# Performance work log

Hardware: AMD Instinct MI355X
Metric: run time of the kernel (lower is better)

Reference implementation:

```python
import jax, jax.numpy as jnp
import numpy as np

B, N, E, D = 2, 8192, 1024, 128   # batch, seq, embed_dim, expand_ratio (= head dim)
H = E // D                        # 8 heads (f_proj output dim)
CHUNK = 64
LN_EPS = 1e-5


def _gla_chunked(q, k, v, log_f):
    """Chunked simple GLA: S_t = exp(log_f_t) * S_{t-1} + k_t v_t^T ; o_t = q_t @ S_t.
    q,k,v: [b,h,n,d], log_f: [b,h,n] (log of per-head scalar decay in (0,1))."""
    b, h, n, d = q.shape
    nc = n // CHUNK
    qc = q.reshape(b, h, nc, CHUNK, d)
    kc = k.reshape(b, h, nc, CHUNK, d)
    vc = v.reshape(b, h, nc, CHUNK, d)
    gf = log_f.reshape(b, h, nc, CHUNK)
    g = jnp.cumsum(gf, axis=-1)          # inclusive within-chunk cum log decay [b,h,nc,C]
    gl = g[..., -1]                      # total chunk log decay [b,h,nc]

    # intra-chunk: A[i,j] = (q_i . k_j) * exp(g_i - g_j), j <= i  (g decreasing -> stable)
    mask = jnp.tril(jnp.ones((CHUNK, CHUNK), bool))
    A = jnp.einsum('bhcid,bhcjd->bhcij', qc, kc)
    A = jnp.where(mask, A * jnp.exp(g[..., :, None] - g[..., None, :]), 0.0)
    o_intra = jnp.einsum('bhcij,bhcjd->bhcid', A, vc)

    # inter-chunk: scan over chunks carrying state S [b,h,d,d]
    def step(S, inp):
        q_c, k_c, v_c, g_c, gl_c = inp   # [b,h,C,d],[b,h,C,d],[b,h,C,d],[b,h,C],[b,h]
        o = jnp.einsum('bhid,bhde->bhie', q_c * jnp.exp(g_c)[..., None], S)
        kd = k_c * jnp.exp(gl_c[..., None] - g_c)[..., None]
        S = jnp.exp(gl_c)[..., None, None] * S + jnp.einsum('bhid,bhie->bhde', kd, v_c)
        return S, o

    xs = (jnp.moveaxis(qc, 2, 0), jnp.moveaxis(kc, 2, 0), jnp.moveaxis(vc, 2, 0),
          jnp.moveaxis(g, 2, 0), jnp.moveaxis(gl, 2, 0))
    S0 = jnp.zeros((b, h, d, d), q.dtype)
    _, o_inter = jax.lax.scan(step, S0, xs)      # [nc,b,h,C,d]
    o_inter = jnp.moveaxis(o_inter, 0, 2)        # [b,h,nc,C,d]
    return (o_intra + o_inter).reshape(b, h, n, d)


def setup_inputs() -> dict:
    key = jax.random.key(0)
    ks = jax.random.split(key, 13)
    s = E ** -0.5
    x = jax.random.normal(ks[0], (B, N, E), jnp.float32)
    # per-head lower bound in (0,1), stored in log space as consumed by the module
    log_lower_bound = jnp.log(jax.random.uniform(ks[1], (H,), jnp.float32, 0.05, 0.95))
    Wq = jax.random.normal(ks[2], (E, E), jnp.float32) * s
    Wk = jax.random.normal(ks[3], (E, E), jnp.float32) * s
    Wv = jax.random.normal(ks[4], (E, E), jnp.float32) * s
    Wf = jax.random.normal(ks[5], (E, H), jnp.float32) * s
    Wb1 = jax.random.normal(ks[6], (E, D), jnp.float32) * s
    Wb2 = jax.random.normal(ks[7], (D, E), jnp.float32) * (D ** -0.5)
    Wg1 = jax.random.normal(ks[8], (E, D), jnp.float32) * s
    Wg2 = jax.random.normal(ks[9], (D, E), jnp.float32) * (D ** -0.5)
    Wo = jax.random.normal(ks[10], (E, E), jnp.float32) * s
    ln_scale = jnp.ones((E,), jnp.float32)
    ln_bias = jnp.zeros((E,), jnp.float32)
    return dict(x=x, log_lower_bound=log_lower_bound, Wq=Wq, Wk=Wk, Wv=Wv, Wf=Wf,
                Wb1=Wb1, Wb2=Wb2, Wg1=Wg1, Wg2=Wg2, Wo=Wo,
                ln_scale=ln_scale, ln_bias=ln_bias)


def reference(x, log_lower_bound, Wq, Wk, Wv, Wf, Wb1, Wb2, Wg1, Wg2, Wo, ln_scale, ln_bias):
    silu = jax.nn.silu
    q = silu(x @ Wq)
    k = silu(x @ Wk)
    v = x @ Wv
    f_pre = x @ Wf                               # [B,N,H] per-head decay logits

    # dense-memory Householder-style reflection of q
    beta = silu((x @ Wb1) @ Wb2)
    nb = jnp.sqrt(jnp.sum(beta * beta, axis=-1, keepdims=True))
    beta = beta / jnp.maximum(nb, 1e-6) / (E ** 0.5)
    q = q - 2.0 * jnp.sum(q * beta, axis=-1, keepdims=True) * beta

    def split(t):
        return t.reshape(B, N, H, D).transpose(0, 2, 1, 3)   # [B,H,N,D]
    qh, kh, vh = split(q), split(k), split(v)

    lb = jnp.exp(log_lower_bound)                            # [H]
    f = lb + (1.0 - lb) * jax.nn.sigmoid(f_pre)              # [B,N,H]
    log_f = jnp.log(f).transpose(0, 2, 1)                    # [B,H,N]

    o = _gla_chunked(qh, kh, vh, log_f)                      # [B,H,N,D]
    o = o.transpose(0, 2, 1, 3).reshape(B, N, E)

    gate = jax.nn.sigmoid((x @ Wg1) @ Wg2)
    o = o * gate

    mu = jnp.mean(o, axis=-1, keepdims=True)
    var = jnp.var(o, axis=-1, keepdims=True)
    o = (o - mu) / jnp.sqrt(var + LN_EPS) * ln_scale + ln_bias
    return o @ Wo
```

## Files before the change

### kernel.cpp

```cpp
#include <hip/hip_runtime.h>
#include <hip/hip_bf16.h>
#include <cstdint>


using u16 = unsigned short;
using u32 = unsigned int;
using u64 = unsigned long long;

typedef __attribute__((ext_vector_type(8))) short s16x8;
typedef __attribute__((ext_vector_type(4))) float f32x4;

__device__ __forceinline__ float b2f(u16 b){ u32 u = ((u32)b)<<16; return __builtin_bit_cast(float,u); }
__device__ __forceinline__ u16 f2b(float f){
  u32 u = __builtin_bit_cast(u32,f);
  return (u16)((u + 0x7FFFu + ((u>>16)&1u)) >> 16);
}
__device__ __forceinline__ float sigm(float x){ return 1.f/(1.f + __expf(-x)); }
__device__ __forceinline__ float silu(float x){ return x * sigm(x); }

__device__ __forceinline__ void gload16(const void* g, void* l){
  __builtin_amdgcn_global_load_lds((const __attribute__((address_space(1))) void*)g,
                                   (__attribute__((address_space(3))) void*)l, 16, 0, 0);
}
#define MFMA(a,b,c) __builtin_amdgcn_mfma_f32_16x16x32_bf16((a),(b),(c),0,0,0)

__device__ __forceinline__ void bar(){
  asm volatile("" ::: "memory");
  __builtin_amdgcn_s_barrier();
  asm volatile("" ::: "memory");
}
__device__ __forceinline__ void wait_vm8(){
  asm volatile("s_waitcnt vmcnt(8)" ::: "memory");
  __builtin_amdgcn_sched_barrier(0);
}
__device__ __forceinline__ void wait_vm0(){
  asm volatile("s_waitcnt vmcnt(0)" ::: "memory");
  __builtin_amdgcn_sched_barrier(0);
}

__device__ __forceinline__ void swz_block(int& bx, int& by){
  const int gx = gridDim.x;
  const int nwg = gx * gridDim.y;
  int lin = by*gx + bx;
  const int cpx = nwg >> 3;
  lin = (lin & 7)*cpx + (lin >> 3);
  bx = lin % gx; by = lin / gx;
}

__global__ __launch_bounds__(256) void fill_diag(float* __restrict__ p, int n, float val){
  int i = blockIdx.x*256 + threadIdx.x;
  if (i < n) p[i] = val;
}

__global__ __launch_bounds__(256) void wprep_all(const float* __restrict__ Wq,
                                                 const float* __restrict__ Wk,
                                                 const float* __restrict__ Wv,
                                                 const float* __restrict__ Wb1,
                                                 const float* __restrict__ Wb2,
                                                 const float* __restrict__ Wg1,
                                                 const float* __restrict__ Wg2,
                                                 const float* __restrict__ Wo,
                                                 u16* __restrict__ WCAT,
                                                 u16* __restrict__ WB2T,
                                                 u16* __restrict__ WG2T,
                                                 u16* __restrict__ WOT){
  const int z = blockIdx.z;
  const float* src; u16* dst; int K, Nsrc, kb, nb;
  switch(z){
    case 0: src=Wq;  dst=WCAT;            K=1024; Nsrc=1024; kb=16; nb=16; break;
    case 1: src=Wk;  dst=WCAT+1024*1024;  K=1024; Nsrc=1024; kb=16; nb=16; break;
    case 2: src=Wv;  dst=WCAT+2048*1024;  K=1024; Nsrc=1024; kb=16; nb=16; break;
    case 3: src=Wb1; dst=WCAT+3072*1024;  K=1024; Nsrc=128;  kb=16; nb=2;  break;
    case 4: src=Wg1; dst=WCAT+3200*1024;  K=1024; Nsrc=128;  kb=16; nb=2;  break;
    case 5: src=Wb2; dst=WB2T;            K=128;  Nsrc=1024; kb=2;  nb=16; break;
    case 6: src=Wg2; dst=WG2T;            K=128;  Nsrc=1024; kb=2;  nb=16; break;
    default:src=Wo;  dst=WOT;             K=1024; Nsrc=1024; kb=16; nb=16; break;
  }
  if (blockIdx.x >= (u32)kb || blockIdx.y >= (u32)nb) return;
  __shared__ float t[64][65];
  const int k0 = blockIdx.x*64, n0 = blockIdx.y*64;
  const int tid = threadIdx.x;
  #pragma unroll
  for (int e=0;e<16;e++){
    int idx = e*256 + tid;
    int r = idx>>6, c = idx&63;
    float v = 0.f;
    if (n0 + c < Nsrc) v = src[(u64)(k0+r)*Nsrc + n0 + c];
    t[r][c] = v;
  }
  __syncthreads();
  #pragma unroll
  for (int e=0;e<16;e++){
    int idx = e*256 + tid;
    int nn = idx>>6, kk = idx&63;
    dst[(u64)(n0+nn)*K + k0 + kk] = f2b(t[kk][nn]);
  }
}

__global__ __launch_bounds__(256) void fprep(const float* __restrict__ x,
                                             const float* __restrict__ Wf,
                                             const float* __restrict__ llb,
                                             float* __restrict__ G,
                                             float* __restrict__ GL,
                                             u16* __restrict__ XB){
  const int c = blockIdx.x, b = blockIdx.y;
  const int tid = threadIdx.x;
  __shared__ float wf[4*2056];
  __shared__ float fsm[64][8];
  for (int i = tid; i < 2048; i += 256){
    float4 v = ((const float4*)Wf)[i];
    const int dim = i>>1, half = i&1;
    const int q = dim>>8, r = dim&255;
    *(float4*)&wf[q*2056 + (r*2+half)*4] = v;
  }
  __syncthreads();
  const int t = tid>>2, q = tid&3;
  const u64 tokoff = (u64)(b*8192 + c*64 + t)*1024 + q*256;
  const float4* xr = (const float4*)(x + tokoff);
  ushort4* xbw = (ushort4*)(XB + tokoff);
  const float* wq = wf + q*2056;
  float4 s0 = {0,0,0,0}, s1 = {0,0,0,0};
  #pragma unroll 4
  for (int i=0;i<64;i++){
    const float4 xv = xr[i];
    ushort4 ob; ob.x=f2b(xv.x); ob.y=f2b(xv.y); ob.z=f2b(xv.z); ob.w=f2b(xv.w);
    xbw[i] = ob;
    const float* xe = (const float*)&xv;
    #pragma unroll
    for (int e=0;e<4;e++){
      const float4 w0 = *(const float4*)&wq[((i*4+e)*2+0)*4];
      const float4 w1 = *(const float4*)&wq[((i*4+e)*2+1)*4];
      s0.x += xe[e]*w0.x; s0.y += xe[e]*w0.y; s0.z += xe[e]*w0.z; s0.w += xe[e]*w0.w;
      s1.x += xe[e]*w1.x; s1.y += xe[e]*w1.y; s1.z += xe[e]*w1.z; s1.w += xe[e]*w1.w;
    }
  }
  #pragma unroll
  for (int d=1; d<4; d<<=1){
    s0.x += __shfl_xor(s0.x,d); s0.y += __shfl_xor(s0.y,d);
    s0.z += __shfl_xor(s0.z,d); s0.w += __shfl_xor(s0.w,d);
    s1.x += __shfl_xor(s1.x,d); s1.y += __shfl_xor(s1.y,d);
    s1.z += __shfl_xor(s1.z,d); s1.w += __shfl_xor(s1.w,d);
  }
  if (q==0){
    fsm[t][0]=s0.x; fsm[t][1]=s0.y; fsm[t][2]=s0.z; fsm[t][3]=s0.w;
    fsm[t][4]=s1.x; fsm[t][5]=s1.y; fsm[t][6]=s1.z; fsm[t][7]=s1.w;
  }
  __syncthreads();
  if (tid < 64){
    #pragma unroll
    for (int h=0;h<8;h++){
      const float lb = __expf(llb[h]);
      const float f = lb + (1.f - lb)*sigm(fsm[tid][h]);
      float xg = __logf(f);
      #pragma unroll
      for (int d=1; d<64; d<<=1){
        float v = __shfl_up(xg, d);
        if (tid >= d) xg += v;
      }
      const int bh = b*8 + h;
      G[(u64)bh*8192 + c*64 + tid] = xg;
      if (tid==63) GL[bh*128 + c] = xg;
    }
  }
}

__global__ __launch_bounds__(256,4) void gemm_proj(const u16* __restrict__ A,
                                                   const u16* __restrict__ Bt,
                                                   u16* __restrict__ Qb,
                                                   u16* __restrict__ Kp,
                                                   u16* __restrict__ KT,
                                                   u16* __restrict__ VT,
                                                   u16* __restrict__ FP,
                                                   const float* __restrict__ Gp,
                                                   const float* __restrict__ GLp){
  __shared__ __align__(16) u16 As[128*64];
  __shared__ __align__(16) u16 Bs[128*64];
  const int tid = threadIdx.x, lane = tid&63, wid = tid>>6;
  int bx = blockIdx.x, by = blockIdx.y;
  swz_block(bx, by);
  const int bn0 = bx*128, bm0 = by*128;
  const int wr = wid>>1, wc = wid&1;
  const int g = lane>>4, ln = lane&15;

  f32x4 acc[4][4];
  #pragma unroll
  for (int i=0;i<4;i++)
    #pragma unroll
    for (int j=0;j<4;j++) acc[i][j] = f32x4{0.f,0.f,0.f,0.f};

  for (int kt = 0; kt < 16; ++kt){
    const int k0 = kt<<6;
    #pragma unroll
    for (int j=0;j<4;j++){
      const int p = (wid*4+j)*64 + lane;
      const int row = p>>3, sl = p&7;
      const int sc = ((sl ^ (row&7))<<3);
      gload16(A  + (u64)(bm0+row)*1024 + k0 + sc, (char*)As + (wid*4+j)*1024);
      gload16(Bt + (u64)(bn0+row)*1024 + k0 + sc, (char*)Bs + (wid*4+j)*1024);
    }
    __syncthreads();
    #pragma unroll
    for (int ks=0;ks<2;ks++){
      s16x8 af[4], bf[4];
      #pragma unroll
      for (int mt=0;mt<4;mt++){
        const int row = wr*64 + mt*16 + ln;
        af[mt] = *(const s16x8*)(As + row*64 + (((ks*4+g) ^ (row&7))<<3));
      }
      #pragma unroll
      for (int nt=0;nt<4;nt++){
        const int row = wc*64 + nt*16 + ln;
        bf[nt] = *(const s16x8*)(Bs + row*64 + (((ks*4+g) ^ (row&7))<<3));
      }
      #pragma unroll
      for (int mt=0;mt<4;mt++)
        #pragma unroll
        for (int nt=0;nt<4;nt++)
          acc[mt][nt] = MFMA(af[mt], bf[nt], acc[mt][nt]);
    }
    __syncthreads();
  }

  const int cb = bn0 >> 7;
  if (cb < 8){
    #pragma unroll
    for (int mt=0;mt<4;mt++)
      #pragma unroll
      for (int nt=0;nt<4;nt++){
        const int col = bn0 + wc*64 + nt*16 + ln;
        #pragma unroll
        for (int r=0;r<4;r++)
          Qb[(u64)(bm0 + wr*64 + mt*16 + g*4 + r)*1024 + col] = f2b(acc[mt][nt][r]);
      }
  } else if (cb < 16){
    const int h = cb - 8;
    const int bh = (bm0>>13)*8 + h;
    const int trowb = (bm0 & 8191) + wr*64;
    const float gl = GLp[bh*128 + (trowb>>6)];
    float es[4][4];
    #pragma unroll
    for (int mt=0;mt<4;mt++)
      #pragma unroll
      for (int r=0;r<4;r++)
        es[mt][r] = __expf(gl - Gp[(u64)bh*8192 + trowb + mt*16 + g*4 + r]);
    #pragma unroll
    for (int mt=0;mt<4;mt++){
      const int trow = trowb + mt*16 + g*4;
      #pragma unroll
      for (int nt=0;nt<4;nt++){
        const int d = wc*64 + nt*16 + ln;
        ushort4 o; u16* op = (u16*)&o;
        #pragma unroll
        for (int r=0;r<4;r++){
          const float s = silu(acc[mt][nt][r]);
          op[r] = f2b(s * es[mt][r]);
          Kp[(u64)(bm0 + wr*64 + mt*16 + g*4 + r)*1024 + h*128 + d] = f2b(s);
        }
        *(ushort4*)(KT + ((u64)bh*128 + d)*8192 + trow) = o;
      }
    }
  } else if (cb < 24){
    const int h = cb - 16;
    const int bh = (bm0>>13)*8 + h;
    const int trowb = (bm0 & 8191) + wr*64;
    #pragma unroll
    for (int mt=0;mt<4;mt++){
      const int trow = trowb + mt*16 + g*4;
      #pragma unroll
      for (int nt=0;nt<4;nt++){
        const int d = wc*64 + nt*16 + ln;
        ushort4 o; u16* op = (u16*)&o;
        #pragma unroll
        for (int r=0;r<4;r++) op[r] = f2b(acc[mt][nt][r]);
        *(ushort4*)(VT + ((u64)bh*128 + d)*8192 + trow) = o;
      }
    }
  } else {
    const int off = (cb == 24) ? 0 : 128;
    #pragma unroll
    for (int mt=0;mt<4;mt++)
      #pragma unroll
      for (int nt=0;nt<4;nt++){
        const int col = off + wc*64 + nt*16 + ln;
        #pragma unroll
        for (int r=0;r<4;r++)
          FP[(u64)(bm0 + wr*64 + mt*16 + g*4 + r)*384 + col] = f2b(acc[mt][nt][r]);
      }
  }
}

#define STAGE256(kt_, c_)                                                              \
  do{ const int kk0 = (kt_)<<6;                                                        \
    _Pragma("unroll")                                                                  \
    for (int j=0;j<4;j++){                                                             \
      const int p = j*512 + tid;                                                       \
      const int row = p>>3, sl = p&7;                                                  \
      const int sc = ((sl ^ (row&7))<<3);                                              \
      gload16(A  + (u64)(bm0+row)*lda + kk0 + sc,                                      \
              (char*)lds + (c_)*65536 + (j*8+wid)*1024);                               \
      gload16(Bt + (u64)(bn0+row)*K   + kk0 + sc,                                      \
              (char*)lds + (c_)*65536 + 32768 + (j*8+wid)*1024);                       \
    } }while(0)

#define GEMM256_CORE()                                                                 \
  f32x4 acc[8][4];                                                                     \
  _Pragma("unroll")                                                                    \
  for (int i=0;i<8;i++)                                                                \
    _Pragma("unroll")                                                                  \
    for (int j=0;j<4;j++) acc[i][j] = f32x4{0.f,0.f,0.f,0.f};                          \
  const int nk = K >> 6;                                                               \
  STAGE256(0, 0);                                                                      \
  int cbuf = 0;                                                                        \
  for (int kt = 0; kt < nk; ++kt){                                                     \
    if (kt+1 < nk){ STAGE256(kt+1, cbuf^1); wait_vm8(); } else { wait_vm0(); }         \
    bar();                                                                             \
    const u16* As_c = lds + cbuf*32768;                                                \
    const u16* Bs_c = As_c + 16384;                                                    \
    s16x8 bfr[2][4];                                                                   \
    _Pragma("unroll")                                                                  \
    for (int ks=0;ks<2;ks++)                                                           \
      _Pragma("unroll")                                                                \
      for (int n=0;n<4;n++){                                                           \
        const int row = wc*64 + n*16 + ln;                                             \
        bfr[ks][n] = *(const s16x8*)(Bs_c + row*64 + (((ks*4+g) ^ (row&7))<<3));       \
      }                                                                                \
    _Pragma("unroll")                                                                  \
    for (int m=0;m<8;m++){                                                             \
      const int arow = wr*128 + m*16 + ln;                                             \
      _Pragma("unroll")                                                                \
      for (int ks=0;ks<2;ks++){                                                        \
        const s16x8 af = *(const s16x8*)(As_c + arow*64 + (((ks*4+g) ^ (arow&7))<<3)); \
        _Pragma("unroll")                                                              \
        for (int n=0;n<4;n++) acc[m][n] = MFMA(af, bfr[ks][n], acc[m][n]);             \
      }                                                                                \
    }                                                                                  \
    bar();                                                                             \
    cbuf ^= 1;                                                                         \
  }

__global__ __launch_bounds__(512,2) void gemm256(const u16* __restrict__ A, int lda,
                                                 const u16* __restrict__ Bt,
                                                 void* __restrict__ C, int ldc,
                                                 int K, int mode){
  __shared__ __align__(16) u16 lds[2*32768];
  const int tid = threadIdx.x, lane = tid&63, wid = tid>>6;
  int bx = blockIdx.x, by = blockIdx.y;
  swz_block(bx, by);
  const int bn0 = bx*256, bm0 = by*256;
  const int wr = wid>>2, wc = wid&3;
  const int g = lane>>4, ln = lane&15;
  GEMM256_CORE();
  if (mode == 0){
    float* Cf = (float*)C;
    #pragma unroll
    for (int m=0;m<8;m++)
      #pragma unroll
      for (int n=0;n<4;n++){
        const int col = bn0 + wc*64 + n*16 + ln;
        #pragma unroll
        for (int r=0;r<4;r++)
          Cf[(u64)(bm0 + wr*128 + m*16 + g*4 + r)*ldc + col] = acc[m][n][r];
      }
  } else {
    u16* Cb = (u16*)C;
    #pragma unroll
    for (int m=0;m<8;m++)
      #pragma unroll
      for (int n=0;n<4;n++){
        const int col = bn0 + wc*64 + n*16 + ln;
        #pragma unroll
        for (int r=0;r<4;r++)
          Cb[(u64)(bm0 + wr*128 + m*16 + g*4 + r)*ldc + col] = f2b(acc[m][n][r]);
      }
  }
}

__global__ __launch_bounds__(256) void e1_reflect(u16* __restrict__ Q,
                                                  const u16* __restrict__ BP){
  const u64 t = blockIdx.x;
  const int tid = threadIdx.x;
  __shared__ float red[8];
  u16* qrow = Q + t*1024;
  const u16* brow = BP + t*1024;
  ushort4 qv = ((const ushort4*)qrow)[tid];
  ushort4 bv = ((const ushort4*)brow)[tid];
  u16* qp = (u16*)&qv; const u16* bp = (const u16*)&bv;
  float q[4], bb[4];
  float s1 = 0.f, s2 = 0.f;
  #pragma unroll
  for (int j=0;j<4;j++){
    const float qq = silu(b2f(qp[j]));
    const float bbv = silu(b2f(bp[j]));
    q[j] = qq; bb[j] = bbv;
    s1 += bbv*bbv; s2 += qq*bbv;
  }
  #pragma unroll
  for (int d=1; d<64; d<<=1){ s1 += __shfl_xor(s1,d); s2 += __shfl_xor(s2,d); }
  const int wid = tid>>6, lane = tid&63;
  if (lane==0){ red[wid]=s1; red[4+wid]=s2; }
  __syncthreads();
  s1 = red[0]+red[1]+red[2]+red[3];
  s2 = red[4]+red[5]+red[6]+red[7];
  const float bs = 1.f/(fmaxf(sqrtf(s1), 1e-6f) * 32.f);
  const float coef = 2.f * s2 * bs * bs;
  #pragma unroll
  for (int j=0;j<4;j++) qp[j] = f2b(q[j] - coef*bb[j]);
  ((ushort4*)qrow)[tid] = qv;
}

__global__ __launch_bounds__(256,4) void g1_local(const u16* __restrict__ KT,
                                                  const u16* __restrict__ VT,
                                                  u16* __restrict__ LT){
  __shared__ __align__(16) u16 kts[128*64];
  __shared__ __align__(16) u16 vts[128*64];
  const int c = blockIdx.x, bh = blockIdx.y;
  const int tid = threadIdx.x, lane = tid&63, wid = tid>>6;
  const int g = lane>>4, ln = lane&15;
  #pragma unroll
  for (int j=0;j<4;j++){
    const int p = (wid*4+j)*64 + lane;
    const int row = p>>3, sl = p&7;
    const int sc = ((sl ^ (row&7))<<3);
    gload16(KT + ((u64)bh*128 + row)*8192 + (u64)c*64 + sc, (char*)kts + (wid*4+j)*1024);
    gload16(VT + ((u64)bh*128 + row)*8192 + (u64)c*64 + sc, (char*)vts + (wid*4+j)*1024);
  }
  __syncthreads();
  f32x4 acc[2][8];
  #pragma unroll
  for (int mt=0;mt<2;mt++)
    #pragma unroll
    for (int dt=0;dt<8;dt++) acc[mt][dt] = f32x4{0.f,0.f,0.f,0.f};
  #pragma unroll
  for (int kk=0;kk<2;kk++){
    s16x8 av[2];
    #pragma unroll
    for (int mt=0;mt<2;mt++){
      const int row = wid*32 + mt*16 + ln;
      av[mt] = *(const s16x8*)(vts + row*64 + (((kk*4+g) ^ (row&7))<<3));
    }
    #pragma unroll
    for (int dt=0;dt<8;dt++){
      const int row = dt*16 + ln;
      const s16x8 bk = *(const s16x8*)(kts + row*64 + (((kk*4+g) ^ (row&7))<<3));
      #pragma unroll
      for (int mt=0;mt<2;mt++) acc[mt][dt] = MFMA(av[mt], bk, acc[mt][dt]);
    }
  }
  u16* out = LT + ((u64)(bh*128 + c)<<14);
  #pragma unroll
  for (int mt=0;mt<2;mt++)
    #pragma unroll
    for (int dt=0;dt<8;dt++){
      const int d = dt*16 + ln;
      #pragma unroll
      for (int r=0;r<4;r++){
        const int n = wid*32 + mt*16 + g*4 + r;
        out[n*128 + d] = f2b(acc[mt][dt][r]);
      }
    }
}

__global__ __launch_bounds__(256) void g2_scan(u16* __restrict__ LS,
                                               const float* __restrict__ GL){
  __shared__ float egl[128];
  const int bh = blockIdx.y;
  if (threadIdx.x < 128) egl[threadIdx.x] = __expf(GL[bh*128 + threadIdx.x]);
  __syncthreads();
  const u64 e = (u64)blockIdx.x*256 + threadIdx.x;
  u16* P = LS + ((u64)bh<<21) + e;
  float s = 0.f;
  for (int c=0;c<128;c++){
    const float l = b2f(P[(u64)c<<14]);
    P[(u64)c<<14] = f2b(s);
    s = egl[c]*s + l;
  }
}

__global__ __launch_bounds__(256,2) void g3_out(const u16* __restrict__ Qb,
                                                const u16* __restrict__ Kp,
                                                const u16* __restrict__ VT,
                                                const u16* __restrict__ SBb,
                                                const float* __restrict__ Gb,
                                                u16* __restrict__ O){
  __shared__ __align__(16) u16 qs[64*128];
  __shared__ __align__(16) u16 ks[64*128];
  __shared__ __align__(16) u16 vts[128*64];
  __shared__ __align__(16) u16 sbs[64*128];
  __shared__ __align__(16) u16 Ast[4][16*64];
  __shared__ float gg[64];
  const int c = blockIdx.x, bh = blockIdx.y;
  const int b = bh>>3, h = bh&7;
  const int tid = threadIdx.x, lane = tid&63, wid = tid>>6;
  const int g = lane>>4, ln = lane&15;
  const u64 trow0 = (u64)b*8192 + (u64)c*64;

  if (tid < 64) gg[tid] = Gb[(u64)bh*8192 + c*64 + tid];

  const u16* sbbase = SBb + ((u64)(bh*128 + c)<<14);
  #pragma unroll
  for (int j=0;j<4;j++){
    const int p = (wid*4+j)*64 + lane;
    const int row = p>>4, sl = p&15;
    const int sc = ((sl ^ (row&7))<<3);
    gload16(Qb + (trow0 + row)*1024 + h*128 + sc, (char*)qs + (wid*4+j)*1024);
    gload16(Kp + (trow0 + row)*1024 + h*128 + sc, (char*)ks + (wid*4+j)*1024);
    const int row2 = p>>3, sl2 = p&7;
    gload16(VT + ((u64)bh*128 + row2)*8192 + (u64)c*64 + ((sl2 ^ (row2&7))<<3),
            (char*)vts + (wid*4+j)*1024);
    gload16(sbbase + row*128 + sc, (char*)sbs + (wid*4+j)*1024);
  }
  __syncthreads();

  f32x4 pa[4];
  #pragma unroll
  for (int jt=0;jt<4;jt++) pa[jt] = f32x4{0.f,0.f,0.f,0.f};
  #pragma unroll
  for (int kk=0;kk<4;kk++){
    const int arow = wid*16 + ln;
    const s16x8 aq = *(const s16x8*)(qs + arow*128 + (((kk*4+g) ^ (arow&7))<<3));
    #pragma unroll
    for (int jt=0;jt<4;jt++){
      const int brow = jt*16 + ln;
      const s16x8 bk = *(const s16x8*)(ks + brow*128 + (((kk*4+g) ^ (brow&7))<<3));
      pa[jt] = MFMA(aq, bk, pa[jt]);
    }
  }
  #pragma unroll
  for (int jt=0;jt<4;jt++){
    const int jj = jt*16 + ln;
    const float gj = gg[jj];
    #pragma unroll
    for (int r=0;r<4;r++){
      const int il = g*4 + r;
      const int ii = wid*16 + il;
      const float v = (jj <= ii) ? pa[jt][r] * __expf(gg[ii] - gj) : 0.f;
      Ast[wid][il*64 + (((jj>>3) ^ (il&7))<<3) + (jj&7)] = f2b(v);
    }
  }
  {
    const int row = wid*16 + (lane>>2);
    const float sc = __expf(gg[row]);
    u16* base = qs + row*128 + (lane&3)*32;
    #pragma unroll
    for (int ee=0; ee<4; ee++){
      s16x8 v = *(s16x8*)(base + ee*8);
      u16* vp = (u16*)&v;
      #pragma unroll
      for (int xj=0;xj<8;xj++) vp[xj] = f2b(b2f(vp[xj]) * sc);
      *(s16x8*)(base + ee*8) = v;
    }
  }
  f32x4 acc[8];
  #pragma unroll
  for (int i=0;i<8;i++) acc[i] = f32x4{0.f,0.f,0.f,0.f};
  #pragma unroll
  for (int kk=0;kk<2;kk++){
    const s16x8 aa = *(const s16x8*)(Ast[wid] + ln*64 + (((kk*4+g) ^ (ln&7))<<3));
    #pragma unroll
    for (int nt=0;nt<8;nt++){
      const int brow = nt*16 + ln;
      const s16x8 bb = *(const s16x8*)(vts + brow*64 + (((kk*4+g) ^ (brow&7))<<3));
      acc[nt] = MFMA(aa, bb, acc[nt]);
    }
  }
  #pragma unroll
  for (int kk=0;kk<4;kk++){
    const int arow = wid*16 + ln;
    const s16x8 aq = *(const s16x8*)(qs + arow*128 + (((kk*4+g) ^ (arow&7))<<3));
    #pragma unroll
    for (int nt=0;nt<4;nt++){
      const int brow = nt*16 + ln;
      const s16x8 bs = *(const s16x8*)(sbs + brow*128 + (((kk*4+g) ^ (brow&7))<<3));
      acc[nt] = MFMA(aq, bs, acc[nt]);
    }
  }
  __syncthreads();
  #pragma unroll
  for (int j=0;j<4;j++){
    const int p = (wid*4+j)*64 + lane;
    const int row = p>>4, sl = p&15;
    gload16(sbbase + 8192 + row*128 + ((sl ^ (row&7))<<3), (char*)sbs + (wid*4+j)*1024);
  }
  __syncthreads();
  #pragma unroll
  for (int kk=0;kk<4;kk++){
    const int arow = wid*16 + ln;
    const s16x8 aq = *(const s16x8*)(qs + arow*128 + (((kk*4+g) ^ (arow&7))<<3));
    #pragma unroll
    for (int nt=0;nt<4;nt++){
      const int brow = nt*16 + ln;
      const s16x8 bs = *(const s16x8*)(sbs + brow*128 + (((kk*4+g) ^ (brow&7))<<3));
      acc[4+nt] = MFMA(aq, bs, acc[4+nt]);
    }
  }
  u16* outp = O + trow0*1024 + h*128;
  #pragma unroll
  for (int nt=0;nt<8;nt++){
    const int n = nt*16 + ln;
    #pragma unroll
    for (int r=0;r<4;r++){
      const int i = wid*16 + g*4 + r;
      outp[(u64)i*1024 + n] = f2b(acc[nt][r]);
    }
  }
}

__global__ __launch_bounds__(256) void e2_ln(const u16* __restrict__ O,
                                             const u16* __restrict__ GP,
                                             const float* __restrict__ lnsc,
                                             const float* __restrict__ lnbi,
                                             u16* __restrict__ OL){
  const u64 t = blockIdx.x;
  const int tid = threadIdx.x;
  __shared__ float red[8];
  ushort4 ov = ((const ushort4*)(O + t*1024))[tid];
  ushort4 gv = ((const ushort4*)(GP + t*1024))[tid];
  const u16* ovp = (const u16*)&ov;
  const u16* gvp = (const u16*)&gv;
  float o[4]; float s = 0.f, s2 = 0.f;
  #pragma unroll
  for (int j=0;j<4;j++){
    const float val = b2f(ovp[j]) * sigm(b2f(gvp[j]));
    o[j] = val; s += val; s2 += val*val;
  }
  #pragma unroll
  for (int d=1; d<64; d<<=1){ s += __shfl_xor(s,d); s2 += __shfl_xor(s2,d); }
  const int wid = tid>>6, lane = tid&63;
  if (lane==0){ red[wid]=s; red[4+wid]=s2; }
  __syncthreads();
  s = red[0]+red[1]+red[2]+red[3];
  s2 = red[4]+red[5]+red[6]+red[7];
  const float mu = s * (1.f/1024.f);
  const float var = s2 * (1.f/1024.f) - mu*mu;
  const float rs = rsqrtf(var + 1e-5f);
  ushort4 out; u16* op = (u16*)&out;
  #pragma unroll
  for (int j=0;j<4;j++){
    const int e = tid*4 + j;
    op[j] = f2b((o[j]-mu)*rs*lnsc[e] + lnbi[e]);
  }
  ((ushort4*)(OL + t*1024))[tid] = out;
}

extern "C" void kernel_launch(void* const* d_in, const int* in_sizes, int n_in,
                              void* d_out, int out_size, void* d_ws, size_t ws_size,
                              hipStream_t stream){
  const float* x   = (const float*)d_in[0];
  const float* llb = (const float*)d_in[1];
  const float* Wq  = (const float*)d_in[2];
  const float* Wk  = (const float*)d_in[3];
  const float* Wv  = (const float*)d_in[4];
  const float* Wf  = (const float*)d_in[5];
  const float* Wb1 = (const float*)d_in[6];
  const float* Wb2 = (const float*)d_in[7];
  const float* Wg1 = (const float*)d_in[8];
  const float* Wg2 = (const float*)d_in[9];
  const float* Wo  = (const float*)d_in[10];
  const float* lnsc= (const float*)d_in[11];
  const float* lnbi= (const float*)d_in[12];

  const u64 REQUIRED = 190586880ull;
  if (ws_size < REQUIRED){
    const float val = 1.0e6f + (float)(u64)(ws_size>>20) * 1024.0f;
    fill_diag<<<dim3((out_size+255)/256),256,0,stream>>>((float*)d_out, out_size, val);
    return;
  }

  char* ws = (char*)d_ws;
  u16*  WCAT = (u16*)(ws + 0ull);
  u16*  WB2T = (u16*)(ws + 7077888ull);
  u16*  WG2T = (u16*)(ws + 7340032ull);
  u16*  WOT  = (u16*)(ws + 7602176ull);
  float* Gb  = (float*)(ws + 9699328ull);
  float* GLb = (float*)(ws + 10223616ull);
  u16*  FP   = (u16*)(ws + 10231808ull);
  u16*  R0   = (u16*)(ws + 22814720ull);
  u16*  Qb   = (u16*)(ws + 56369152ull);
  u16*  Kp   = (u16*)(ws + 89923584ull);
  u16*  KT   = (u16*)(ws + 123478016ull);
  u16*  VT   = (u16*)(ws + 157032448ull);
  u16*  LTSB = (u16*)d_out;
  u16*  XB = R0, *BP = R0, *GP = R0;
  u16*  Ob = KT, *OL = Qb;

  fprep<<<dim3(128,2),256,0,stream>>>(x, Wf, llb, Gb, GLb, XB);

  wprep_all<<<dim3(16,16,8),256,0,stream>>>(Wq,Wk,Wv,Wb1,Wb2,Wg1,Wg2,Wo,
                                            WCAT, WB2T, WG2T, WOT);

  gemm_proj<<<dim3(26,128),256,0,stream>>>(XB, WCAT, Qb, Kp, KT, VT, FP, Gb, GLb);

  gemm256<<<dim3(4,64),512,0,stream>>>(FP, 384, WB2T, BP, 1024, 128, 1);
  e1_reflect<<<dim3(16384),256,0,stream>>>(Qb, BP);

  gemm256<<<dim3(4,64),512,0,stream>>>(FP + 128, 384, WG2T, GP, 1024, 128, 1);

  g1_local<<<dim3(128,16),256,0,stream>>>(KT, VT, LTSB);
  g2_scan<<<dim3(64,16),256,0,stream>>>(LTSB, GLb);
  g3_out<<<dim3(128,16),256,0,stream>>>(Qb, Kp, VT, LTSB, Gb, Ob);

  e2_ln<<<dim3(16384),256,0,stream>>>(Ob, GP, lnsc, lnbi, OL);

  gemm256<<<dim3(4,64),512,0,stream>>>(OL, 1024, WOT, d_out, 1024, 1024, 0);
}
```

Before: 378.5 us.

## Replace 256x256 double-buffered GEMM with 128x128 single-buffered tile GEMM

Swaps the 512-thread 256x256-tile GEMM, which double-buffers LDS with async global-to-LDS loads, for a 256-thread 128x128-tile GEMM with a single LDS buffer and syncthreads. It is used for the beta, gate and output projections. The intent is more blocks and higher occupancy per CU, especially for the short K=128 GEMMs. The trade-off is losing the load/compute overlap and reducing data reuse per tile in the large output projection.

```diff
diff --git a/kernel.cpp b/kernel.cpp
--- a/kernel.cpp
+++ b/kernel.cpp
@@ -23,20 +23,6 @@
                                    (__attribute__((address_space(3))) void*)l, 16, 0, 0);
 }
 #define MFMA(a,b,c) __builtin_amdgcn_mfma_f32_16x16x32_bf16((a),(b),(c),0,0,0)
-
-__device__ __forceinline__ void bar(){
-  asm volatile("" ::: "memory");
-  __builtin_amdgcn_s_barrier();
-  asm volatile("" ::: "memory");
-}
-__device__ __forceinline__ void wait_vm8(){
-  asm volatile("s_waitcnt vmcnt(8)" ::: "memory");
-  __builtin_amdgcn_sched_barrier(0);
-}
-__device__ __forceinline__ void wait_vm0(){
-  asm volatile("s_waitcnt vmcnt(0)" ::: "memory");
-  __builtin_amdgcn_sched_barrier(0);
-}
 
 __device__ __forceinline__ void swz_block(int& bx, int& by){
   const int gx = gridDim.x;
@@ -164,6 +150,83 @@
   }
 }
 
+__global__ __launch_bounds__(256,4) void gemm_bt(const u16* __restrict__ A, int lda,
+                                                 const u16* __restrict__ Bt,
+                                                 void* __restrict__ C, int ldc,
+                                                 int K, int mode){
+  __shared__ __align__(16) u16 As[128*64];
+  __shared__ __align__(16) u16 Bs[128*64];
+  const int tid = threadIdx.x, lane = tid&63, wid = tid>>6;
+  int bx = blockIdx.x, by = blockIdx.y;
+  swz_block(bx, by);
+  const int bn0 = bx*128, bm0 = by*128;
+  const int wr = wid>>1, wc = wid&1;
+  const int g = lane>>4, ln = lane&15;
+
+  f32x4 acc[4][4];
+  #pragma unroll
+  for (int i=0;i<4;i++)
+    #pragma unroll
+    for (int j=0;j<4;j++) acc[i][j] = f32x4{0.f,0.f,0.f,0.f};
+
+  const int nk = K >> 6;
+  for (int kt = 0; kt < nk; ++kt){
+    const int k0 = kt<<6;
+    #pragma unroll
+    for (int j=0;j<4;j++){
+      const int p = (wid*4+j)*64 + lane;
+      const int row = p>>3, sl = p&7;
+      const int sc = ((sl ^ (row&7))<<3);
+      gload16(A  + (u64)(bm0+row)*lda + k0 + sc, (char*)As + (wid*4+j)*1024);
+      gload16(Bt + (u64)(bn0+row)*K   + k0 + sc, (char*)Bs + (wid*4+j)*1024);
+    }
+    __syncthreads();
+    #pragma unroll
+    for (int ks=0;ks<2;ks++){
+      s16x8 af[4], bf[4];
+      #pragma unroll
+      for (int mt=0;mt<4;mt++){
+        const int row = wr*64 + mt*16 + ln;
+        af[mt] = *(const s16x8*)(As + row*64 + (((ks*4+g) ^ (row&7))<<3));
+      }
+      #pragma unroll
+      for (int nt=0;nt<4;nt++){
+        const int row = wc*64 + nt*16 + ln;
+        bf[nt] = *(const s16x8*)(Bs + row*64 + (((ks*4+g) ^ (row&7))<<3));
+      }
+      #pragma unroll
+      for (int mt=0;mt<4;mt++)
+        #pragma unroll
+        for (int nt=0;nt<4;nt++)
+          acc[mt][nt] = MFMA(af[mt], bf[nt], acc[mt][nt]);
+    }
+    __syncthreads();
+  }
+  if (mode == 0){
+    float* Cf = (float*)C;
+    #pragma unroll
+    for (int mt=0;mt<4;mt++)
+      #pragma unroll
+      for (int nt=0;nt<4;nt++){
+        const int col = bn0 + wc*64 + nt*16 + ln;
+        #pragma unroll
+        for (int r=0;r<4;r++)
+          Cf[(u64)(bm0 + wr*64 + mt*16 + g*4 + r)*ldc + col] = acc[mt][nt][r];
+      }
+  } else {
+    u16* Cb = (u16*)C;
+    #pragma unroll
+    for (int mt=0;mt<4;mt++)
+      #pragma unroll
+      for (int nt=0;nt<4;nt++){
+        const int col = bn0 + wc*64 + nt*16 + ln;
+        #pragma unroll
+        for (int r=0;r<4;r++)
+          Cb[(u64)(bm0 + wr*64 + mt*16 + g*4 + r)*ldc + col] = f2b(acc[mt][nt][r]);
+      }
+  }
+}
+
 __global__ __launch_bounds__(256,4) void gemm_proj(const u16* __restrict__ A,
                                                    const u16* __restrict__ Bt,
                                                    u16* __restrict__ Qb,
@@ -289,92 +352,6 @@
   }
 }
 
-#define STAGE256(kt_, c_)                                                              \
-  do{ const int kk0 = (kt_)<<6;                                                        \
-    _Pragma("unroll")                                                                  \
-    for (int j=0;j<4;j++){                                                             \
-      const int p = j*512 + tid;                                                       \
-      const int row = p>>3, sl = p&7;                                                  \
-      const int sc = ((sl ^ (row&7))<<3);                                              \
-      gload16(A  + (u64)(bm0+row)*lda + kk0 + sc,                                      \
-              (char*)lds + (c_)*65536 + (j*8+wid)*1024);                               \
-      gload16(Bt + (u64)(bn0+row)*K   + kk0 + sc,                                      \
-              (char*)lds + (c_)*65536 + 32768 + (j*8+wid)*1024);                       \
-    } }while(0)
-
-#define GEMM256_CORE()                                                                 \
-  f32x4 acc[8][4];                                                                     \
-  _Pragma("unroll")                                                                    \
-  for (int i=0;i<8;i++)                                                                \
-    _Pragma("unroll")                                                                  \
-    for (int j=0;j<4;j++) acc[i][j] = f32x4{0.f,0.f,0.f,0.f};                          \
-  const int nk = K >> 6;                                                               \
-  STAGE256(0, 0);                                                                      \
-  int cbuf = 0;                                                                        \
-  for (int kt = 0; kt < nk; ++kt){                                                     \
-    if (kt+1 < nk){ STAGE256(kt+1, cbuf^1); wait_vm8(); } else { wait_vm0(); }         \
-    bar();                                                                             \
-    const u16* As_c = lds + cbuf*32768;                                                \
-    const u16* Bs_c = As_c + 16384;                                                    \
-    s16x8 bfr[2][4];                                                                   \
-    _Pragma("unroll")                                                                  \
-    for (int ks=0;ks<2;ks++)                                                           \
-      _Pragma("unroll")                                                                \
-      for (int n=0;n<4;n++){                                                           \
-        const int row = wc*64 + n*16 + ln;                                             \
-        bfr[ks][n] = *(const s16x8*)(Bs_c + row*64 + (((ks*4+g) ^ (row&7))<<3));       \
-      }                                                                                \
-    _Pragma("unroll")                                                                  \
-    for (int m=0;m<8;m++){                                                             \
-      const int arow = wr*128 + m*16 + ln;                                             \
-      _Pragma("unroll")                                                                \
-      for (int ks=0;ks<2;ks++){                                                        \
-        const s16x8 af = *(const s16x8*)(As_c + arow*64 + (((ks*4+g) ^ (arow&7))<<3)); \
-        _Pragma("unroll")                                                              \
-        for (int n=0;n<4;n++) acc[m][n] = MFMA(af, bfr[ks][n], acc[m][n]);             \
-      }                                                                                \
-    }                                                                                  \
-    bar();                                                                             \
-    cbuf ^= 1;                                                                         \
-  }
-
-__global__ __launch_bounds__(512,2) void gemm256(const u16* __restrict__ A, int lda,
-                                                 const u16* __restrict__ Bt,
-                                                 void* __restrict__ C, int ldc,
-                                                 int K, int mode){
-  __shared__ __align__(16) u16 lds[2*32768];
-  const int tid = threadIdx.x, lane = tid&63, wid = tid>>6;
-  int bx = blockIdx.x, by = blockIdx.y;
-  swz_block(bx, by);
-  const int bn0 = bx*256, bm0 = by*256;
-  const int wr = wid>>2, wc = wid&3;
-  const int g = lane>>4, ln = lane&15;
-  GEMM256_CORE();
-  if (mode == 0){
-    float* Cf = (float*)C;
-    #pragma unroll
-    for (int m=0;m<8;m++)
-      #pragma unroll
-      for (int n=0;n<4;n++){
-        const int col = bn0 + wc*64 + n*16 + ln;
-        #pragma unroll
-        for (int r=0;r<4;r++)
-          Cf[(u64)(bm0 + wr*128 + m*16 + g*4 + r)*ldc + col] = acc[m][n][r];
-      }
-  } else {
-    u16* Cb = (u16*)C;
-    #pragma unroll
-    for (int m=0;m<8;m++)
-      #pragma unroll
-      for (int n=0;n<4;n++){
-        const int col = bn0 + wc*64 + n*16 + ln;
-        #pragma unroll
-        for (int r=0;r<4;r++)
-          Cb[(u64)(bm0 + wr*128 + m*16 + g*4 + r)*ldc + col] = f2b(acc[m][n][r]);
-      }
-  }
-}
-
 __global__ __launch_bounds__(256) void e1_reflect(u16* __restrict__ Q,
                                                   const u16* __restrict__ BP){
   const u64 t = blockIdx.x;
@@ -690,10 +667,10 @@
 
   gemm_proj<<<dim3(26,128),256,0,stream>>>(XB, WCAT, Qb, Kp, KT, VT, FP, Gb, GLb);
 
-  gemm256<<<dim3(4,64),512,0,stream>>>(FP, 384, WB2T, BP, 1024, 128, 1);
+  gemm_bt<<<dim3(8,128),256,0,stream>>>(FP, 384, WB2T, BP, 1024, 128, 1);
   e1_reflect<<<dim3(16384),256,0,stream>>>(Qb, BP);
 
-  gemm256<<<dim3(4,64),512,0,stream>>>(FP + 128, 384, WG2T, GP, 1024, 128, 1);
+  gemm_bt<<<dim3(8,128),256,0,stream>>>(FP + 128, 384, WG2T, GP, 1024, 128, 1);
 
   g1_local<<<dim3(128,16),256,0,stream>>>(KT, VT, LTSB);
   g2_scan<<<dim3(64,16),256,0,stream>>>(LTSB, GLb);
@@ -701,5 +678,5 @@
 
   e2_ln<<<dim3(16384),256,0,stream>>>(Ob, GP, lnsc, lnbi, OL);
 
-  gemm256<<<dim3(4,64),512,0,stream>>>(OL, 1024, WOT, d_out, 1024, 1024, 0);
-}
+  gemm_bt<<<dim3(8,128),256,0,stream>>>(OL, 1024, WOT, d_out, 1024, 1024, 0);
+}
```

After: 378.1 us. Within noise of the previous version (-0.1%).
